# Performance work log

Hardware: AMD Instinct MI355X
Metric: run time of the kernel (lower is better)

The kernel has to match this reference:

```python
import jax, jax.numpy as jnp
import numpy as np

DIM_U1 = 20
DIM_U2 = 20
DZ = 6
BATCH = 4096


def _mlp(x, Wa, ba, Wb, bb, Wc, bc, Wd, bd):
    h = jax.nn.relu(x @ Wa + ba)
    h = jax.nn.relu(h @ Wb + bb)
    h = jax.nn.relu(h @ Wc + bc)
    return h @ Wd + bd


def setup_inputs() -> dict:
    key = jax.random.key(0)
    ks = jax.random.split(key, 9)

    def lin(k, fan_in, fan_out):
        k1, k2 = jax.random.split(k)
        lim = 1.0 / np.sqrt(fan_in)
        W = jax.random.uniform(k1, (fan_in, fan_out), minval=-lim, maxval=lim, dtype=jnp.float32)
        b = jax.random.uniform(k2, (fan_out,), minval=-lim, maxval=lim, dtype=jnp.float32)
        return W, b

    d = {"x": jax.random.normal(ks[0], (BATCH, DIM_U1), dtype=jnp.float32)}
    dims1 = [(3, 16), (16, 32), (32, 16), (16, 1 + DZ * 3)]
    dims2 = [(3, 16), (16, 32), (32, 16), (16, DZ + 5 * DZ * DZ)]
    names = ["a", "b", "c", "d"]
    for j, (fi, fo) in enumerate(dims1):
        W, b = lin(ks[1 + j], fi, fo)
        d["W1" + names[j]] = W
        d["b1" + names[j]] = b
    for j, (fi, fo) in enumerate(dims2):
        W, b = lin(ks[5 + j], fi, fo)
        d["W2" + names[j]] = W
        d["b2" + names[j]] = b
    return d


def reference(x, W1a, b1a, W1b, b1b, W1c, b1c, W1d, b1d,
              W2a, b2a, W2b, b2b, W2c, b2c, W2d, b2d):
    B = x.shape[0]
    # gather local neighbor triples: [B, dim_u1, 3]
    idx = (jnp.arange(DIM_U1)[:, None] + jnp.arange(-1, 2)[None, :]) % DIM_U1
    xl = x[:, idx]
    out1 = _mlp(xl, W1a, b1a, W1b, b1b, W1c, b1c, W1d, b1d)  # [B, 20, 19]
    out2 = _mlp(xl, W2a, b2a, W2b, b2b, W2c, b2c, W2d, b2d)  # [B, 20, 186]

    f1 = out1[:, :, :1]  # [B, 20, 1]

    # banded scatter for g1: [B, dim_u1, dz*dim_u2]
    rows1 = jnp.arange(DIM_U1)[:, None]
    cols1 = (jnp.arange(3 * DZ)[None, :] + (jnp.arange(DIM_U1)[:, None] - 1) * DZ) % (DZ * DIM_U2)
    g1 = jnp.zeros((B, DIM_U1, DZ * DIM_U2), x.dtype).at[:, rows1, cols1].set(out1[:, :, 1:])

    f2 = out2[:, :, :DZ].reshape(B, DZ * DIM_U2, 1)

    # banded scatter for g2: [B, dz*dim_u2, dz*dim_u2]
    rows2 = jnp.arange(DZ * DIM_U2)[:, None]
    base = (jnp.arange(5 * DZ)[None, :] + (jnp.arange(DIM_U2)[:, None] - 2) * DZ) % (DZ * DIM_U2)  # [20, 30]
    cols2 = jnp.repeat(base, DZ, axis=0)  # [120, 30]
    vals2 = out2[:, :, DZ:].reshape(B, DZ * DIM_U2, 5 * DZ)
    g2 = jnp.zeros((B, DZ * DIM_U2, DZ * DIM_U2), x.dtype).at[:, rows2, cols2].set(vals2)

    return (f1, g1, f2, g2)
```

## Files before the change

kernel.cpp:

```cpp
#include <hip/hip_runtime.h>

typedef unsigned short u16;
typedef unsigned int   u32;

#define U 20

struct Ptrs { const float* p[16]; };

static __device__ __forceinline__ float bf2f(u16 h) {
    u32 u = ((u32)h) << 16;
    float f;
    __builtin_memcpy(&f, &u, 4);
    return f;
}

static __device__ __forceinline__ u16 f2bf(float f) {
    u32 u;
    __builtin_memcpy(&u, &f, 4);
    u32 lsb = (u >> 16) & 1u;
    u += 0x7fffu + lsb;
    return (u16)(u >> 16);
}

static __device__ __forceinline__ u32 pack2(float a, float b) {
    return (u32)f2bf(a) | ((u32)f2bf(b) << 16);
}

static __device__ __forceinline__ float gr(float f) { return bf2f(f2bf(f)); }

__launch_bounds__(256)
__global__ void mlp_k(const float* __restrict__ x, Ptrs pt,
                      u32* __restrict__ ws, int T) {
    const int t = blockIdx.x * 256 + threadIdx.x;
    if (t >= T) return;
    const int b = t / U;
    const int i = t - b * U;

    const float* W1a = pt.p[0];  const float* b1a = pt.p[1];
    const float* W1b = pt.p[2];  const float* b1b = pt.p[3];
    const float* W1c = pt.p[4];  const float* b1c = pt.p[5];
    const float* W1d = pt.p[6];  const float* b1d = pt.p[7];
    const float* W2a = pt.p[8];  const float* b2a = pt.p[9];
    const float* W2b = pt.p[10]; const float* b2b = pt.p[11];
    const float* W2c = pt.p[12]; const float* b2c = pt.p[13];
    const float* W2d = pt.p[14]; const float* b2d = pt.p[15];

    const float* xb = x + (size_t)b * U;
    int im = (i == 0)     ? U - 1 : i - 1;
    int ip = (i == U - 1) ? 0     : i + 1;
    float v0 = xb[im], v1 = xb[i], v2 = xb[ip];

    float h1[16], h2[32], h3[16];

    #pragma unroll
    for (int n = 0; n < 16; n++)
        h1[n] = fmaxf(b1a[n] + v0 * W1a[n] + v1 * W1a[16 + n] + v2 * W1a[32 + n], 0.f);

    #pragma unroll
    for (int n = 0; n < 32; n++) h2[n] = b1b[n];
    #pragma unroll
    for (int k = 0; k < 16; k++) {
        float hk = h1[k];
        #pragma unroll
        for (int n = 0; n < 32; n++) h2[n] += hk * W1b[k * 32 + n];
    }
    #pragma unroll
    for (int n = 0; n < 32; n++) h2[n] = fmaxf(h2[n], 0.f);

    #pragma unroll
    for (int n = 0; n < 16; n++) h3[n] = b1c[n];
    #pragma unroll
    for (int k = 0; k < 32; k++) {
        float hk = h2[k];
        #pragma unroll
        for (int n = 0; n < 16; n++) h3[n] += hk * W1c[k * 16 + n];
    }
    #pragma unroll
    for (int n = 0; n < 16; n++) h3[n] = fmaxf(h3[n], 0.f);

    {
        float o1[19];
        #pragma unroll
        for (int n = 0; n < 19; n++) o1[n] = b1d[n];
        #pragma unroll
        for (int k = 0; k < 16; k++) {
            float hk = h3[k];
            #pragma unroll
            for (int n = 0; n < 19; n++) o1[n] += hk * W1d[k * 19 + n];
        }
        #pragma unroll
        for (int m = 0; m < 9; m++)
            ws[(size_t)m * T + t] = pack2(o1[2 * m], o1[2 * m + 1]);
        ws[(size_t)9 * T + t] = pack2(o1[18], 0.f);
    }

    #pragma unroll
    for (int n = 0; n < 16; n++)
        h1[n] = fmaxf(b2a[n] + v0 * W2a[n] + v1 * W2a[16 + n] + v2 * W2a[32 + n], 0.f);

    #pragma unroll
    for (int n = 0; n < 32; n++) h2[n] = b2b[n];
    #pragma unroll
    for (int k = 0; k < 16; k++) {
        float hk = h1[k];
        #pragma unroll
        for (int n = 0; n < 32; n++) h2[n] += hk * W2b[k * 32 + n];
    }
    #pragma unroll
    for (int n = 0; n < 32; n++) h2[n] = fmaxf(h2[n], 0.f);

    #pragma unroll
    for (int n = 0; n < 16; n++) h3[n] = b2c[n];
    #pragma unroll
    for (int k = 0; k < 32; k++) {
        float hk = h2[k];
        #pragma unroll
        for (int n = 0; n < 16; n++) h3[n] += hk * W2c[k * 16 + n];
    }
    #pragma unroll
    for (int n = 0; n < 16; n++) h3[n] = fmaxf(h3[n], 0.f);

    {
        float o2a[6];
        #pragma unroll
        for (int n = 0; n < 6; n++) o2a[n] = b2d[n];
        #pragma unroll
        for (int k = 0; k < 16; k++) {
            float hk = h3[k];
            #pragma unroll
            for (int n = 0; n < 6; n++) o2a[n] += hk * W2d[k * 186 + n];
        }
        ws[(size_t)10 * T + t] = pack2(o2a[0], o2a[1]);
        ws[(size_t)11 * T + t] = pack2(o2a[2], o2a[3]);
        ws[(size_t)12 * T + t] = pack2(o2a[4], o2a[5]);
    }

    for (int z = 0; z < 6; z++) {
        float o2[30];
        #pragma unroll
        for (int n = 0; n < 30; n++) o2[n] = b2d[6 + z * 30 + n];
        #pragma unroll
        for (int k = 0; k < 16; k++) {
            float hk = h3[k];
            #pragma unroll
            for (int n = 0; n < 30; n++) o2[n] += hk * W2d[k * 186 + 6 + z * 30 + n];
        }
        #pragma unroll
        for (int m = 0; m < 15; m++)
            ws[(size_t)(13 + z * 15 + m) * T + t] = pack2(o2[2 * m], o2[2 * m + 1]);
    }
}

__launch_bounds__(256)
__global__ void scatter_k(const u32* __restrict__ ws, float* __restrict__ out,
                          int B) {
    __shared__ __align__(16) u16 s1[20 * 20];
    __shared__ __align__(16) u16 s2[20 * 186];
    const int tid = threadIdx.x;
    const int b   = blockIdx.x;
    const int T   = B * U;

    for (int idx = tid; idx < 2060; idx += 256) {
        int n2 = idx / 20;
        int w  = idx - n2 * 20;
        u32 v = ws[(size_t)n2 * T + b * 20 + w];
        if (n2 < 10) {
            *reinterpret_cast<u32*>(&s1[w * 20 + n2 * 2]) = v;
        } else {
            int np = n2 - 10;
            *reinterpret_cast<u32*>(&s2[w * 186 + np * 2]) = v;
        }
    }
    __syncthreads();

    const size_t g1_off = (size_t)B * 20;
    const size_t f2_off = (size_t)B * 2420;
    const size_t g2_off = (size_t)B * 2540;

    float4* og2 = reinterpret_cast<float4*>(out + g2_off + (size_t)b * 14400);
    float4* og1 = reinterpret_cast<float4*>(out + g1_off + (size_t)b * 2400);
    float4* of2 = reinterpret_cast<float4*>(out + f2_off + (size_t)b * 120);
    float4* of1 = reinterpret_cast<float4*>(out + (size_t)b * 20);

    for (int idx = tid; idx < 4235; idx += 256) {
        float vp[4];
        if (idx < 3600) {
            int q  = idx;
            int r  = q / 30, c4 = q - r * 30;
            int i  = r / 6,  z  = r - i * 6;
            int s0 = (i >= 2 ? (i - 2) : (i + 18)) * 6;
            int d0 = 4 * c4 - s0; if (d0 < 0) d0 += 120;
            const u16* src = &s2[i * 186 + 6 + z * 30];
            #pragma unroll
            for (int k = 0; k < 4; k++) {
                int d = d0 + k; if (d >= 120) d -= 120;
                vp[k] = (d < 30) ? bf2f(src[d]) : 0.f;
            }
            float4 v; v.x = vp[0]; v.y = vp[1]; v.z = vp[2]; v.w = vp[3];
            og2[q] = v;
        } else if (idx < 4200) {
            int q  = idx - 3600;
            int i  = q / 30, c4 = q - i * 30;
            int s0 = (i >= 1 ? (i - 1) : 19) * 6;
            int d0 = 4 * c4 - s0; if (d0 < 0) d0 += 120;
            const u16* src = &s1[i * 20 + 1];
            #pragma unroll
            for (int k = 0; k < 4; k++) {
                int d = d0 + k; if (d >= 120) d -= 120;
                vp[k] = (d < 18) ? bf2f(src[d]) : 0.f;
            }
            float4 v; v.x = vp[0]; v.y = vp[1]; v.z = vp[2]; v.w = vp[3];
            og1[q] = v;
        } else if (idx < 4230) {
            int q = idx - 4200;
            #pragma unroll
            for (int k = 0; k < 4; k++) {
                int f = 4 * q + k;
                int i = f / 6, zz = f - i * 6;
                vp[k] = bf2f(s2[i * 186 + zz]);
            }
            float4 v; v.x = vp[0]; v.y = vp[1]; v.z = vp[2]; v.w = vp[3];
            of2[q] = v;
        } else {
            int q = idx - 4230;
            #pragma unroll
            for (int k = 0; k < 4; k++)
                vp[k] = bf2f(s1[(4 * q + k) * 20]);
            float4 v; v.x = vp[0]; v.y = vp[1]; v.z = vp[2]; v.w = vp[3];
            of1[q] = v;
        }
    }
}

__launch_bounds__(256)
__global__ void fused(const float* __restrict__ x, Ptrs pt,
                      float* __restrict__ out, int B) {
    __shared__ __align__(16) float lds[16940];
    const int tid = threadIdx.x;
    const int b   = blockIdx.x;

    float* s_f1 = lds;
    float* s_f2 = lds + 20;
    float* s_g1 = lds + 140;
    float* s_g2 = lds + 2540;

    const int  i = tid >> 3;
    const int  s = tid & 7;
    float v0 = 0.f, v1 = 0.f, v2 = 0.f;
    if (tid < 160) {
        const float* xb = x + (size_t)b * U;
        int im = (i == 0)     ? U - 1 : i - 1;
        int ip = (i == U - 1) ? 0     : i + 1;
        v0 = xb[im]; v1 = xb[i]; v2 = xb[ip];
    }

    {
        float4 z; z.x = z.y = z.z = z.w = 0.f;
        float4* zp = reinterpret_cast<float4*>(s_g1);
        #pragma unroll
        for (int it = 0; it < 17; ++it) {
            int idx = it * 256 + tid;
            if (idx < 4200) zp[idx] = z;
        }
    }
    __syncthreads();

    if (tid < 160) {
        float h1[16], h2[32], h3[16];

        if (s == 0) {
            const float* W1a = pt.p[0];  const float* b1a = pt.p[1];
            const float* W1b = pt.p[2];  const float* b1b = pt.p[3];
            const float* W1c = pt.p[4];  const float* b1c = pt.p[5];
            const float* W1d = pt.p[6];  const float* b1d = pt.p[7];

            #pragma unroll
            for (int n = 0; n < 16; n++)
                h1[n] = fmaxf(b1a[n] + v0 * W1a[n] + v1 * W1a[16 + n] + v2 * W1a[32 + n], 0.f);

            #pragma unroll
            for (int n = 0; n < 32; n++) h2[n] = b1b[n];
            #pragma unroll
            for (int k = 0; k < 16; k++) {
                float hk = h1[k];
                #pragma unroll
                for (int n = 0; n < 32; n++) h2[n] += hk * W1b[k * 32 + n];
            }
            #pragma unroll
            for (int n = 0; n < 32; n++) h2[n] = fmaxf(h2[n], 0.f);

            #pragma unroll
            for (int n = 0; n < 16; n++) h3[n] = b1c[n];
            #pragma unroll
            for (int k = 0; k < 32; k++) {
                float hk = h2[k];
                #pragma unroll
                for (int n = 0; n < 16; n++) h3[n] += hk * W1c[k * 16 + n];
            }
            #pragma unroll
            for (int n = 0; n < 16; n++) h3[n] = fmaxf(h3[n], 0.f);

            float o1[19];
            #pragma unroll
            for (int n = 0; n < 19; n++) o1[n] = b1d[n];
            #pragma unroll
            for (int k = 0; k < 16; k++) {
                float hk = h3[k];
                #pragma unroll
                for (int n = 0; n < 19; n++) o1[n] += hk * W1d[k * 19 + n];
            }
            s_f1[i] = gr(o1[0]);
            float* row = s_g1 + i * 120;
            #pragma unroll
            for (int j = 0; j < 3; j++) {
                int cc = i - 1 + j;
                if (cc < 0)  cc += U;
                if (cc >= U) cc -= U;
                float2* d = reinterpret_cast<float2*>(row + cc * 6);
                #pragma unroll
                for (int m = 0; m < 3; m++) {
                    float2 v; v.x = gr(o1[1 + j * 6 + 2 * m]);
                              v.y = gr(o1[1 + j * 6 + 2 * m + 1]);
                    d[m] = v;
                }
            }
        } else {
            const float* W2a = pt.p[8];  const float* b2a = pt.p[9];
            const float* W2b = pt.p[10]; const float* b2b = pt.p[11];
            const float* W2c = pt.p[12]; const float* b2c = pt.p[13];
            const float* W2d = pt.p[14]; const float* b2d = pt.p[15];

            #pragma unroll
            for (int n = 0; n < 16; n++)
                h1[n] = fmaxf(b2a[n] + v0 * W2a[n] + v1 * W2a[16 + n] + v2 * W2a[32 + n], 0.f);

            #pragma unroll
            for (int n = 0; n < 32; n++) h2[n] = b2b[n];
            #pragma unroll
            for (int k = 0; k < 16; k++) {
                float hk = h1[k];
                #pragma unroll
                for (int n = 0; n < 32; n++) h2[n] += hk * W2b[k * 32 + n];
            }
            #pragma unroll
            for (int n = 0; n < 32; n++) h2[n] = fmaxf(h2[n], 0.f);

            #pragma unroll
            for (int n = 0; n < 16; n++) h3[n] = b2c[n];
            #pragma unroll
            for (int k = 0; k < 32; k++) {
                float hk = h2[k];
                #pragma unroll
                for (int n = 0; n < 16; n++) h3[n] += hk * W2c[k * 16 + n];
            }
            #pragma unroll
            for (int n = 0; n < 16; n++) h3[n] = fmaxf(h3[n], 0.f);

            if (s == 1) {
                float o2a[6];
                #pragma unroll
                for (int n = 0; n < 6; n++) o2a[n] = b2d[n];
                #pragma unroll
                for (int k = 0; k < 16; k++) {
                    float hk = h3[k];
                    #pragma unroll
                    for (int n = 0; n < 6; n++) o2a[n] += hk * W2d[k * 186 + n];
                }
                float2* d = reinterpret_cast<float2*>(s_f2 + i * 6);
                #pragma unroll
                for (int m = 0; m < 3; m++) {
                    float2 v; v.x = gr(o2a[2 * m]); v.y = gr(o2a[2 * m + 1]);
                    d[m] = v;
                }
            } else {
                const int z = s - 2;
                float o2[30];
                #pragma unroll
                for (int n = 0; n < 30; n++) o2[n] = b2d[6 + z * 30 + n];
                #pragma unroll
                for (int k = 0; k < 16; k++) {
                    float hk = h3[k];
                    #pragma unroll
                    for (int n = 0; n < 30; n++) o2[n] += hk * W2d[k * 186 + 6 + z * 30 + n];
                }
                float* row = s_g2 + (i * 6 + z) * 120;
                #pragma unroll
                for (int j = 0; j < 5; j++) {
                    int cc = i - 2 + j;
                    if (cc < 0)  cc += U;
                    if (cc >= U) cc -= U;
                    float2* d = reinterpret_cast<float2*>(row + cc * 6);
                    #pragma unroll
                    for (int m = 0; m < 3; m++) {
                        float2 v; v.x = gr(o2[j * 6 + 2 * m]);
                                  v.y = gr(o2[j * 6 + 2 * m + 1]);
                        d[m] = v;
                    }
                }
            }
        }
    }
    __syncthreads();

    const size_t g1_off = (size_t)B * 20;
    const size_t f2_off = (size_t)B * 2420;
    const size_t g2_off = (size_t)B * 2540;

    {
        const float4* sp = reinterpret_cast<const float4*>(s_g2);
        float4* dp = reinterpret_cast<float4*>(out + g2_off + (size_t)b * 14400);
        #pragma unroll
        for (int it = 0; it < 15; ++it) {
            int idx = it * 256 + tid;
            if (idx < 3600) dp[idx] = sp[idx];
        }
    }
    {
        const float4* sp = reinterpret_cast<const float4*>(s_g1);
        float4* dp = reinterpret_cast<float4*>(out + g1_off + (size_t)b * 2400);
        #pragma unroll
        for (int it = 0; it < 3; ++it) {
            int idx = it * 256 + tid;
            if (idx < 600) dp[idx] = sp[idx];
        }
    }
    if (tid < 5) {
        const float4* sp = reinterpret_cast<const float4*>(s_f1);
        float4* dp = reinterpret_cast<float4*>(out + (size_t)b * 20);
        dp[tid] = sp[tid];
    }
    {
        int q = tid - 64;
        if (q >= 0 && q < 30) {
            const float4* sp = reinterpret_cast<const float4*>(s_f2);
            float4* dp = reinterpret_cast<float4*>(out + f2_off + (size_t)b * 120);
            dp[q] = sp[q];
        }
    }
}

extern "C" void kernel_launch(void* const* d_in, const int* in_sizes, int n_in,
                              void* d_out, int out_size, void* d_ws, size_t ws_size,
                              hipStream_t stream) {
    const float* x = (const float*)d_in[0];
    Ptrs pt;
    for (int a = 0; a < 16; a++) pt.p[a] = (const float*)d_in[1 + a];

    int total = in_sizes[0];
    int B = total / U;
    int T = total;

    size_t need = (size_t)103 * (size_t)T * 4;
    if (d_ws != nullptr && ws_size >= need) {
        u32* ws = (u32*)d_ws;
        int blocks1 = (T + 255) / 256;
        mlp_k<<<blocks1, 256, 0, stream>>>(x, pt, ws, T);
        scatter_k<<<B, 256, 0, stream>>>(ws, (float*)d_out, B);
    } else {
        fused<<<B, 256, 0, stream>>>(x, pt, (float*)d_out, B);
    }
}
```

Before: 419.4 us.

## Stage MLP weights in LDS and split the two MLPs across half-blocks

The MLP kernel now copies all weights and biases into shared memory, padding the output-layer rows, instead of reading them from global memory. Each block covers 128 positions, with the first half of its threads computing MLP1 and the second half computing MLP2, which shortens the per-thread critical path. The costs are a per-block weight load, a barrier, twice as many blocks, and uneven work between the halves, since MLP2 is much larger and the two halves sit in different waves.

```diff
diff --git a/kernel.cpp b/kernel.cpp
--- a/kernel.cpp
+++ b/kernel.cpp
@@ -31,19 +31,41 @@
 __launch_bounds__(256)
 __global__ void mlp_k(const float* __restrict__ x, Ptrs pt,
                       u32* __restrict__ ws, int T) {
-    const int t = blockIdx.x * 256 + threadIdx.x;
-    if (t >= T) return;
-    const int b = t / U;
-    const int i = t - b * U;
-
-    const float* W1a = pt.p[0];  const float* b1a = pt.p[1];
-    const float* W1b = pt.p[2];  const float* b1b = pt.p[3];
-    const float* W1c = pt.p[4];  const float* b1c = pt.p[5];
-    const float* W1d = pt.p[6];  const float* b1d = pt.p[7];
-    const float* W2a = pt.p[8];  const float* b2a = pt.p[9];
-    const float* W2b = pt.p[10]; const float* b2b = pt.p[11];
-    const float* W2c = pt.p[12]; const float* b2c = pt.p[13];
-    const float* W2d = pt.p[14]; const float* b2d = pt.p[15];
+    __shared__ __align__(16) float wl[5824];
+    const int tid = threadIdx.x;
+
+    {
+        const float* srcs[14] = { pt.p[0], pt.p[1], pt.p[2], pt.p[3], pt.p[4],
+                                  pt.p[5], pt.p[7],
+                                  pt.p[8], pt.p[9], pt.p[10], pt.p[11],
+                                  pt.p[12], pt.p[13], pt.p[15] };
+        const int offs[14] = { 0, 48, 64, 576, 608, 1120, 1456,
+                               1488, 1536, 1552, 2064, 2096, 2608, 5632 };
+        const int cnts[14] = { 48, 16, 512, 32, 512, 16, 19,
+                               48, 16, 512, 32, 512, 16, 186 };
+        #pragma unroll
+        for (int a = 0; a < 14; a++) {
+            const float* s = srcs[a];
+            const int off = offs[a], c = cnts[a];
+            for (int idx = tid; idx < c; idx += 256)
+                wl[off + idx] = s[idx];
+        }
+        for (int idx = tid; idx < 304; idx += 256) {
+            int r = idx / 19, cl = idx - r * 19;
+            wl[1136 + r * 20 + cl] = pt.p[6][idx];
+        }
+        for (int idx = tid; idx < 2976; idx += 256) {
+            int r = idx / 186, cl = idx - r * 186;
+            wl[2624 + r * 188 + cl] = pt.p[14][idx];
+        }
+    }
+    __syncthreads();
+
+    const int tt    = blockIdx.x * 128 + (tid & 127);
+    const int which = tid >> 7;
+    if (tt >= T) return;
+    const int b = tt / U;
+    const int i = tt - b * U;
 
     const float* xb = x + (size_t)b * U;
     int im = (i == 0)     ? U - 1 : i - 1;
@@ -52,102 +74,112 @@
 
     float h1[16], h2[32], h3[16];
 
-    #pragma unroll
-    for (int n = 0; n < 16; n++)
-        h1[n] = fmaxf(b1a[n] + v0 * W1a[n] + v1 * W1a[16 + n] + v2 * W1a[32 + n], 0.f);
-
-    #pragma unroll
-    for (int n = 0; n < 32; n++) h2[n] = b1b[n];
-    #pragma unroll
-    for (int k = 0; k < 16; k++) {
-        float hk = h1[k];
-        #pragma unroll
-        for (int n = 0; n < 32; n++) h2[n] += hk * W1b[k * 32 + n];
-    }
-    #pragma unroll
-    for (int n = 0; n < 32; n++) h2[n] = fmaxf(h2[n], 0.f);
-
-    #pragma unroll
-    for (int n = 0; n < 16; n++) h3[n] = b1c[n];
-    #pragma unroll
-    for (int k = 0; k < 32; k++) {
-        float hk = h2[k];
-        #pragma unroll
-        for (int n = 0; n < 16; n++) h3[n] += hk * W1c[k * 16 + n];
-    }
-    #pragma unroll
-    for (int n = 0; n < 16; n++) h3[n] = fmaxf(h3[n], 0.f);
-
-    {
+    if (which == 0) {
+        const float* Wa = &wl[0];    const float* ba = &wl[48];
+        const float* Wb = &wl[64];   const float* bb = &wl[576];
+        const float* Wc = &wl[608];  const float* bc = &wl[1120];
+        const float* Wd = &wl[1136]; const float* bd = &wl[1456];
+
+        #pragma unroll
+        for (int n = 0; n < 16; n++)
+            h1[n] = fmaxf(ba[n] + v0 * Wa[n] + v1 * Wa[16 + n] + v2 * Wa[32 + n], 0.f);
+
+        #pragma unroll
+        for (int n = 0; n < 32; n++) h2[n] = bb[n];
+        #pragma unroll
+        for (int k = 0; k < 16; k++) {
+            float hk = h1[k];
+            #pragma unroll
+            for (int n = 0; n < 32; n++) h2[n] += hk * Wb[k * 32 + n];
+        }
+        #pragma unroll
+        for (int n = 0; n < 32; n++) h2[n] = fmaxf(h2[n], 0.f);
+
+        #pragma unroll
+        for (int n = 0; n < 16; n++) h3[n] = bc[n];
+        #pragma unroll
+        for (int k = 0; k < 32; k++) {
+            float hk = h2[k];
+            #pragma unroll
+            for (int n = 0; n < 16; n++) h3[n] += hk * Wc[k * 16 + n];
+        }
+        #pragma unroll
+        for (int n = 0; n < 16; n++) h3[n] = fmaxf(h3[n], 0.f);
+
         float o1[19];
         #pragma unroll
-        for (int n = 0; n < 19; n++) o1[n] = b1d[n];
+        for (int n = 0; n < 19; n++) o1[n] = bd[n];
         #pragma unroll
         for (int k = 0; k < 16; k++) {
             float hk = h3[k];
             #pragma unroll
-            for (int n = 0; n < 19; n++) o1[n] += hk * W1d[k * 19 + n];
+            for (int n = 0; n < 19; n++) o1[n] += hk * Wd[k * 20 + n];
         }
         #pragma unroll
         for (int m = 0; m < 9; m++)
-            ws[(size_t)m * T + t] = pack2(o1[2 * m], o1[2 * m + 1]);
-        ws[(size_t)9 * T + t] = pack2(o1[18], 0.f);
-    }
-
-    #pragma unroll
-    for (int n = 0; n < 16; n++)
-        h1[n] = fmaxf(b2a[n] + v0 * W2a[n] + v1 * W2a[16 + n] + v2 * W2a[32 + n], 0.f);
-
-    #pragma unroll
-    for (int n = 0; n < 32; n++) h2[n] = b2b[n];
-    #pragma unroll
-    for (int k = 0; k < 16; k++) {
-        float hk = h1[k];
-        #pragma unroll
-        for (int n = 0; n < 32; n++) h2[n] += hk * W2b[k * 32 + n];
-    }
-    #pragma unroll
-    for (int n = 0; n < 32; n++) h2[n] = fmaxf(h2[n], 0.f);
-
-    #pragma unroll
-    for (int n = 0; n < 16; n++) h3[n] = b2c[n];
-    #pragma unroll
-    for (int k = 0; k < 32; k++) {
-        float hk = h2[k];
-        #pragma unroll
-        for (int n = 0; n < 16; n++) h3[n] += hk * W2c[k * 16 + n];
-    }
-    #pragma unroll
-    for (int n = 0; n < 16; n++) h3[n] = fmaxf(h3[n], 0.f);
-
-    {
-        float o2a[6];
-        #pragma unroll
-        for (int n = 0; n < 6; n++) o2a[n] = b2d[n];
+            ws[(size_t)m * T + tt] = pack2(o1[2 * m], o1[2 * m + 1]);
+        ws[(size_t)9 * T + tt] = pack2(o1[18], 0.f);
+    } else {
+        const float* Wa = &wl[1488]; const float* ba = &wl[1536];
+        const float* Wb = &wl[1552]; const float* bb = &wl[2064];
+        const float* Wc = &wl[2096]; const float* bc = &wl[2608];
+        const float* Wd = &wl[2624]; const float* bd = &wl[5632];
+
+        #pragma unroll
+        for (int n = 0; n < 16; n++)
+            h1[n] = fmaxf(ba[n] + v0 * Wa[n] + v1 * Wa[16 + n] + v2 * Wa[32 + n], 0.f);
+
+        #pragma unroll
+        for (int n = 0; n < 32; n++) h2[n] = bb[n];
         #pragma unroll
         for (int k = 0; k < 16; k++) {
-            float hk = h3[k];
-            #pragma unroll
-            for (int n = 0; n < 6; n++) o2a[n] += hk * W2d[k * 186 + n];
-        }
-        ws[(size_t)10 * T + t] = pack2(o2a[0], o2a[1]);
-        ws[(size_t)11 * T + t] = pack2(o2a[2], o2a[3]);
-        ws[(size_t)12 * T + t] = pack2(o2a[4], o2a[5]);
-    }
-
-    for (int z = 0; z < 6; z++) {
-        float o2[30];
-        #pragma unroll
-        for (int n = 0; n < 30; n++) o2[n] = b2d[6 + z * 30 + n];
-        #pragma unroll
-        for (int k = 0; k < 16; k++) {
-            float hk = h3[k];
-            #pragma unroll
-            for (int n = 0; n < 30; n++) o2[n] += hk * W2d[k * 186 + 6 + z * 30 + n];
-        }
-        #pragma unroll
-        for (int m = 0; m < 15; m++)
-            ws[(size_t)(13 + z * 15 + m) * T + t] = pack2(o2[2 * m], o2[2 * m + 1]);
+            float hk = h1[k];
+            #pragma unroll
+            for (int n = 0; n < 32; n++) h2[n] += hk * Wb[k * 32 + n];
+        }
+        #pragma unroll
+        for (int n = 0; n < 32; n++) h2[n] = fmaxf(h2[n], 0.f);
+
+        #pragma unroll
+        for (int n = 0; n < 16; n++) h3[n] = bc[n];
+        #pragma unroll
+        for (int k = 0; k < 32; k++) {
+            float hk = h2[k];
+            #pragma unroll
+            for (int n = 0; n < 16; n++) h3[n] += hk * Wc[k * 16 + n];
+        }
+        #pragma unroll
+        for (int n = 0; n < 16; n++) h3[n] = fmaxf(h3[n], 0.f);
+
+        {
+            float o2a[6];
+            #pragma unroll
+            for (int n = 0; n < 6; n++) o2a[n] = bd[n];
+            #pragma unroll
+            for (int k = 0; k < 16; k++) {
+                float hk = h3[k];
+                #pragma unroll
+                for (int n = 0; n < 6; n++) o2a[n] += hk * Wd[k * 188 + n];
+            }
+            ws[(size_t)10 * T + tt] = pack2(o2a[0], o2a[1]);
+            ws[(size_t)11 * T + tt] = pack2(o2a[2], o2a[3]);
+            ws[(size_t)12 * T + tt] = pack2(o2a[4], o2a[5]);
+        }
+
+        for (int z = 0; z < 6; z++) {
+            float o2[30];
+            #pragma unroll
+            for (int n = 0; n < 30; n++) o2[n] = bd[6 + z * 30 + n];
+            #pragma unroll
+            for (int k = 0; k < 16; k++) {
+                float hk = h3[k];
+                #pragma unroll
+                for (int n = 0; n < 30; n++) o2[n] += hk * Wd[k * 188 + 6 + z * 30 + n];
+            }
+            #pragma unroll
+            for (int m = 0; m < 15; m++)
+                ws[(size_t)(13 + z * 15 + m) * T + tt] = pack2(o2[2 * m], o2[2 * m + 1]);
+        }
     }
 }
 
@@ -453,7 +485,7 @@
     size_t need = (size_t)103 * (size_t)T * 4;
     if (d_ws != nullptr && ws_size >= need) {
         u32* ws = (u32*)d_ws;
-        int blocks1 = (T + 255) / 256;
+        int blocks1 = (T + 127) / 128;
         mlp_k<<<blocks1, 256, 0, stream>>>(x, pt, ws, T);
         scatter_k<<<B, 256, 0, stream>>>(ws, (float*)d_out, B);
     } else {
```

New measurement: 369.9 us (median of 2 runs). 1.13x faster.
